# Kernel tuning notes

Hardware: AMD Instinct MI355X
Metric: run time of the kernel (lower is better)

The kernel has to match this reference:

```python
import jax, jax.numpy as jnp
import numpy as np

N_NODES = 50000
N_EDGES = 800000
IN_DIM = 96
OUT_DIM = 96
EDGE_DIM = 32
BN_EPS = 1e-5


def setup_inputs() -> dict:
    key = jax.random.key(0)
    ks = jax.random.split(key, 12)
    x = jax.random.normal(ks[0], (N_NODES, IN_DIM), dtype=jnp.float32)
    edge_index = jax.random.randint(ks[1], (2, N_EDGES), 0, N_NODES, dtype=jnp.int64)
    edge_attr = jax.random.normal(ks[2], (N_EDGES, EDGE_DIM), dtype=jnp.float32)
    # GINEConv edge projection Linear(edge_dim, in_dim)
    We = jax.random.normal(ks[3], (EDGE_DIM, IN_DIM), dtype=jnp.float32) / np.sqrt(EDGE_DIM)
    be = jnp.zeros((IN_DIM,), dtype=jnp.float32)
    # MLP: Linear(in_dim, out_dim) -> ReLU -> Linear(out_dim, out_dim)
    W1 = jax.random.normal(ks[4], (IN_DIM, OUT_DIM), dtype=jnp.float32) / np.sqrt(IN_DIM)
    b1 = jnp.zeros((OUT_DIM,), dtype=jnp.float32)
    W2 = jax.random.normal(ks[5], (OUT_DIM, OUT_DIM), dtype=jnp.float32) / np.sqrt(OUT_DIM)
    b2 = jnp.zeros((OUT_DIM,), dtype=jnp.float32)
    # BatchNorm1d affine params
    gamma = jnp.ones((OUT_DIM,), dtype=jnp.float32)
    beta = jnp.zeros((OUT_DIM,), dtype=jnp.float32)
    return {"x": x, "edge_index": edge_index, "edge_attr": edge_attr,
            "We": We, "be": be, "W1": W1, "b1": b1, "W2": W2, "b2": b2,
            "gamma": gamma, "beta": beta}


def reference(x, edge_index, edge_attr, We, be, W1, b1, W2, b2, gamma, beta):
    src = edge_index[0]  # x_j (message source)
    dst = edge_index[1]  # aggregation target
    # GINE message: ReLU(x_j + Lin(edge_attr)) per edge  [E, in_dim]
    msg = jax.nn.relu(x[src] + edge_attr @ We + be)
    # sum aggregation into dst nodes  [N, in_dim]
    aggr = jax.ops.segment_sum(msg, dst, num_segments=x.shape[0])
    # (1 + eps) * x + aggr, eps = 0 (GINEConv default)
    h = x + aggr
    # MLP: Linear -> ReLU -> Linear
    h = jax.nn.relu(h @ W1 + b1) @ W2 + b2
    # BatchNorm1d (training-mode batch statistics) + affine
    mean = jnp.mean(h, axis=0)
    var = jnp.mean(jnp.square(h - mean), axis=0)  # biased var, as torch BN uses
    h = (h - mean) * jax.lax.rsqrt(var + BN_EPS) * gamma + beta
    # ReLU (dropout is identity in eval / deterministic reference)
    return jax.nn.relu(h)
```

## Files before the change

kernel.cpp:

```cpp
#include <hip/hip_runtime.h>

typedef unsigned short ushort_t;
typedef unsigned int uint_t;
typedef __attribute__((ext_vector_type(8))) short bf16x8;
typedef __attribute__((ext_vector_type(4))) float f32x4;
typedef __attribute__((ext_vector_type(2))) float f32x2;

#define N_NODES 50000
#define N_EDGES 800000
#define BN_EPS 1e-5f

#define OFF_STATS 4800000
#define OFF_FLAG  4800192

#define SC_PAIR  0
#define SC_LEXCL 1600000
#define SC_DEG   1650016
#define SC_RANK  1700032
#define SC_BSUM  2500032

#define NB_SCAN 196
#define MTILE 64
#define NTILES ((N_NODES + MTILE - 1) / MTILE)

__device__ __forceinline__ ushort_t f2bf(float f) {
    uint_t u = __float_as_uint(f);
    uint_t r = ((u >> 16) & 1u) + 0x7fffu;
    return (ushort_t)((u + r) >> 16);
}

__global__ __launch_bounds__(256) void init_kernel(const int* __restrict__ ei,
                                                   int* __restrict__ flag,
                                                   int* __restrict__ deg,
                                                   float* __restrict__ stats) {
    const int gtid = blockIdx.x * 256 + threadIdx.x;
    const int nth = gridDim.x * 256;
    for (int i = gtid; i < N_NODES; i += nth) deg[i] = 0;
    if (gtid < 256) stats[gtid] = 0.f;
    if (blockIdx.x == 0) {
        __shared__ int s_any;
        if (threadIdx.x == 0) s_any = 0;
        __syncthreads();
        int nz = 0;
#pragma unroll
        for (int j = 0; j < 16; ++j) {
            const int p = 1 + 2 * (threadIdx.x * 16 + j) * 195;
            if (ei[p] != 0) nz = 1;
        }
        if (nz) atomicOr(&s_any, 1);
        __syncthreads();
        if (threadIdx.x == 0) *flag = s_any ? 0 : 1;
    }
}

__global__ __launch_bounds__(256) void hist_kernel(const int* __restrict__ ei,
                                                   const int* __restrict__ flag,
                                                   int* __restrict__ deg,
                                                   int* __restrict__ rank) {
    const int is64 = *flag;
    const int stride = gridDim.x * blockDim.x;
    for (int e = blockIdx.x * blockDim.x + threadIdx.x; e < N_EDGES; e += stride) {
        int s, d;
        if (is64) { s = ei[2 * e]; d = ei[2 * N_EDGES + 2 * e]; }
        else      { s = ei[e];     d = ei[N_EDGES + e]; }
        if ((uint_t)s < N_NODES && (uint_t)d < N_NODES)
            rank[e] = atomicAdd(&deg[d], 1);
    }
}

__global__ __launch_bounds__(256) void scanA_kernel(const int* __restrict__ deg,
                                                    int* __restrict__ lexcl,
                                                    int* __restrict__ bsum) {
    __shared__ int sd[256];
    const int tid = threadIdx.x;
    const int i = blockIdx.x * 256 + tid;
    const int v = (i < N_NODES) ? deg[i] : 0;
    sd[tid] = v;
    __syncthreads();
    for (int off = 1; off < 256; off <<= 1) {
        int u = (tid >= off) ? sd[tid - off] : 0;
        __syncthreads();
        sd[tid] += u;
        __syncthreads();
    }
    if (i < N_NODES) lexcl[i] = sd[tid] - v;
    if (tid == 255) bsum[blockIdx.x] = sd[255];
}

__device__ __forceinline__ void build_sbase(const int* __restrict__ bsum,
                                            int* sd, int* sbase, int* tot) {
    const int tid = threadIdx.x;
    const int v = (tid < NB_SCAN) ? bsum[tid] : 0;
    sd[tid] = v;
    __syncthreads();
    for (int off = 1; off < 256; off <<= 1) {
        int u = (tid >= off) ? sd[tid - off] : 0;
        __syncthreads();
        sd[tid] += u;
        __syncthreads();
    }
    if (tid < NB_SCAN) sbase[tid] = sd[tid] - v;
    if (tid == NB_SCAN - 1) *tot = sd[tid];
    __syncthreads();
}

__global__ __launch_bounds__(256) void scatter_kernel(const int* __restrict__ ei,
                                                      const int* __restrict__ flag,
                                                      const int* __restrict__ lexcl,
                                                      const int* __restrict__ bsum,
                                                      const int* __restrict__ rank,
                                                      int2* __restrict__ pair) {
    __shared__ int sd[256];
    __shared__ int sbase[NB_SCAN];
    __shared__ int tot;
    build_sbase(bsum, sd, sbase, &tot);

    const int is64 = *flag;
    const int stride = gridDim.x * blockDim.x;
    for (int e = blockIdx.x * blockDim.x + threadIdx.x; e < N_EDGES; e += stride) {
        int s, d;
        if (is64) { s = ei[2 * e]; d = ei[2 * N_EDGES + 2 * e]; }
        else      { s = ei[e];     d = ei[N_EDGES + e]; }
        if ((uint_t)s < N_NODES && (uint_t)d < N_NODES) {
            const int pos = sbase[d >> 8] + lexcl[d] + rank[e];
            pair[pos] = make_int2(e, s);
        }
    }
}

__global__ __launch_bounds__(256) void node_aggr_kernel(
    const float* __restrict__ x, const float* __restrict__ ea,
    const float* __restrict__ We, const float* __restrict__ be,
    const int2* __restrict__ pair, const int* __restrict__ lexcl,
    const int* __restrict__ bsum, float* __restrict__ hbuf) {
    __shared__ int sd[256];
    __shared__ int sbase[NB_SCAN];
    __shared__ int tot;
    build_sbase(bsum, sd, sbase, &tot);

    const int lane = threadIdx.x & 63;
    const int q = lane >> 4;
    const int t = lane & 15;
    const int wav = blockIdx.x * 4 + (threadIdx.x >> 6);
    const int nwav = gridDim.x * 4;

    bf16x8 Bf[6];
    float ben[6];
#pragma unroll
    for (int f = 0; f < 6; ++f) {
        const int n = t + 16 * f;
#pragma unroll
        for (int j = 0; j < 8; ++j) {
            const int k = q * 8 + j;
            Bf[f][j] = (short)f2bf(We[k * 96 + n]);
        }
        ben[f] = be[n];
    }

    for (int n = wav; n < N_NODES; n += nwav) {
        const int off = sbase[n >> 8] + lexcl[n];
        const int offn = (n + 1 == N_NODES) ? tot
                         : sbase[(n + 1) >> 8] + lexcl[n + 1];
        const int deg = offn - off;

        float part[6];
#pragma unroll
        for (int f = 0; f < 6; ++f) part[f] = 0.f;

        for (int c0 = 0; c0 < deg; c0 += 16) {
            const int rem = deg - c0;
            int eid_t = -1, src_t = -1;
            if (t < rem) {
                const int2 p = pair[off + c0 + t];
                eid_t = p.x;
                src_t = p.y;
            }
            bf16x8 A = {0, 0, 0, 0, 0, 0, 0, 0};
            if (eid_t >= 0) {
                const float* row = ea + (size_t)eid_t * 32 + q * 8;
                f32x4 a0 = *(const f32x4*)(row);
                f32x4 a1 = *(const f32x4*)(row + 4);
#pragma unroll
                for (int j = 0; j < 4; ++j) {
                    A[j] = (short)f2bf(a0[j]);
                    A[4 + j] = (short)f2bf(a1[j]);
                }
            }

            f32x4 acc[6];
#pragma unroll
            for (int f = 0; f < 6; ++f) {
                f32x4 z = {0.f, 0.f, 0.f, 0.f};
                acc[f] = __builtin_amdgcn_mfma_f32_16x16x32_bf16(A, Bf[f], z, 0, 0, 0);
            }

            int s_r[4];
#pragma unroll
            for (int r = 0; r < 4; ++r) s_r[r] = __shfl(src_t, q * 4 + r);

#pragma unroll
            for (int r = 0; r < 4; ++r) {
                const int m = q * 4 + r;
                if (m < rem) {
                    const float* xrow = x + (size_t)s_r[r] * 96;
#pragma unroll
                    for (int f = 0; f < 6; ++f) {
                        float v = acc[f][r] + ben[f] + xrow[t + 16 * f];
                        part[f] += v > 0.f ? v : 0.f;
                    }
                }
            }
        }

#pragma unroll
        for (int f = 0; f < 6; ++f) {
            part[f] += __shfl_xor(part[f], 16);
            part[f] += __shfl_xor(part[f], 32);
        }

        if (q == 0) {
            const float* xn = x + (size_t)n * 96;
            float* hn = hbuf + (size_t)n * 96;
#pragma unroll
            for (int f = 0; f < 6; ++f) {
                const int col = t + 16 * f;
                hn[col] = part[f] + xn[col];
            }
        }
    }
}

__global__ __launch_bounds__(256) void mlp_kernel(
    float* buf, const float* __restrict__ W1g, const float* __restrict__ b1g,
    const float* __restrict__ W2g, const float* __restrict__ b2g,
    float* __restrict__ stats) {
    __shared__ float Ws[96 * 96];
    __shared__ float hsT[96][68];

    const int tid = threadIdx.x;
    const int fg = tid & 15;
    const int ng = tid >> 4;
    const int n0 = blockIdx.x * MTILE;

    for (int i = tid; i < 96 * 96 / 4; i += 256)
        ((f32x4*)Ws)[i] = ((const f32x4*)W1g)[i];
    for (int i = tid; i < MTILE * 96 / 4; i += 256) {
        const int base = i * 4;
        const int nn = base / 96, k = base - nn * 96;
        f32x4 v = {0.f, 0.f, 0.f, 0.f};
        if (n0 + nn < N_NODES)
            v = *(const f32x4*)(buf + (size_t)(n0 + nn) * 96 + k);
        hsT[k][nn] = v[0]; hsT[k + 1][nn] = v[1];
        hsT[k + 2][nn] = v[2]; hsT[k + 3][nn] = v[3];
    }
    __syncthreads();

    float acc[4][6];
#pragma unroll
    for (int ff = 0; ff < 6; ++ff) {
        const float b = b1g[6 * fg + ff];
        acc[0][ff] = b; acc[1][ff] = b; acc[2][ff] = b; acc[3][ff] = b;
    }
    for (int k = 0; k < 96; ++k) {
        const f32x4 a = *(const f32x4*)&hsT[k][4 * ng];
        const float* wr = &Ws[k * 96 + 6 * fg];
        const f32x2 w01 = *(const f32x2*)(wr);
        const f32x2 w23 = *(const f32x2*)(wr + 2);
        const f32x2 w45 = *(const f32x2*)(wr + 4);
        const float w[6] = {w01[0], w01[1], w23[0], w23[1], w45[0], w45[1]};
#pragma unroll
        for (int nn = 0; nn < 4; ++nn)
#pragma unroll
            for (int ff = 0; ff < 6; ++ff) acc[nn][ff] += a[nn] * w[ff];
    }
    __syncthreads();

#pragma unroll
    for (int nn = 0; nn < 4; ++nn)
#pragma unroll
        for (int ff = 0; ff < 6; ++ff) {
            float v = acc[nn][ff];
            hsT[6 * fg + ff][4 * ng + nn] = v > 0.f ? v : 0.f;
        }
    for (int i = tid; i < 96 * 96 / 4; i += 256)
        ((f32x4*)Ws)[i] = ((const f32x4*)W2g)[i];
    __syncthreads();

#pragma unroll
    for (int ff = 0; ff < 6; ++ff) {
        const float b = b2g[6 * fg + ff];
        acc[0][ff] = b; acc[1][ff] = b; acc[2][ff] = b; acc[3][ff] = b;
    }
    for (int k = 0; k < 96; ++k) {
        const f32x4 a = *(const f32x4*)&hsT[k][4 * ng];
        const float* wr = &Ws[k * 96 + 6 * fg];
        const f32x2 w01 = *(const f32x2*)(wr);
        const f32x2 w23 = *(const f32x2*)(wr + 2);
        const f32x2 w45 = *(const f32x2*)(wr + 4);
        const float w[6] = {w01[0], w01[1], w23[0], w23[1], w45[0], w45[1]};
#pragma unroll
        for (int nn = 0; nn < 4; ++nn)
#pragma unroll
            for (int ff = 0; ff < 6; ++ff) acc[nn][ff] += a[nn] * w[ff];
    }

#pragma unroll
    for (int nn = 0; nn < 4; ++nn) {
        const int n = n0 + 4 * ng + nn;
        if (n < N_NODES) {
            float* o = buf + (size_t)n * 96 + 6 * fg;
            *(f32x2*)(o)     = (f32x2){acc[nn][0], acc[nn][1]};
            *(f32x2*)(o + 2) = (f32x2){acc[nn][2], acc[nn][3]};
            *(f32x2*)(o + 4) = (f32x2){acc[nn][4], acc[nn][5]};
        }
    }

    __syncthreads();
#pragma unroll
    for (int nn = 0; nn < 4; ++nn)
#pragma unroll
        for (int ff = 0; ff < 6; ++ff)
            hsT[6 * fg + ff][4 * ng + nn] = acc[nn][ff];
    __syncthreads();

    if (tid < 96) {
        int nmax = N_NODES - n0;
        if (nmax > MTILE) nmax = MTILE;
        float s = 0.f, s2 = 0.f;
        for (int n = 0; n < nmax; ++n) {
            const float v = hsT[tid][n];
            s += v; s2 += v * v;
        }
        atomicAdd(&stats[tid], s);
        atomicAdd(&stats[96 + tid], s2);
    }
}

__global__ __launch_bounds__(256) void bn_kernel(
    const float* __restrict__ h2, const float* __restrict__ stats,
    const float* __restrict__ gamma, const float* __restrict__ beta,
    float* __restrict__ out) {
    __shared__ float sc[96], sh[96];
    const int tid = threadIdx.x;
    if (tid < 96) {
        const float inv_n = 1.f / (float)N_NODES;
        const float mean = stats[tid] * inv_n;
        float var = stats[96 + tid] * inv_n - mean * mean;
        var = var > 0.f ? var : 0.f;
        const float s = gamma[tid] * rsqrtf(var + BN_EPS);
        sc[tid] = s;
        sh[tid] = beta[tid] - mean * s;
    }
    __syncthreads();
    const int total4 = N_NODES * 96 / 4;
    for (int i = blockIdx.x * blockDim.x + tid; i < total4;
         i += gridDim.x * blockDim.x) {
        f32x4 v = ((const f32x4*)h2)[i];
        const int jb = (i * 4) % 96;
#pragma unroll
        for (int c = 0; c < 4; ++c) {
            float u = v[c] * sc[jb + c] + sh[jb + c];
            v[c] = u > 0.f ? u : 0.f;
        }
        ((f32x4*)out)[i] = v;
    }
}

extern "C" void kernel_launch(void* const* d_in, const int* in_sizes, int n_in,
                              void* d_out, int out_size, void* d_ws,
                              size_t ws_size, hipStream_t stream) {
    const float* x     = (const float*)d_in[0];
    const int*   ei    = (const int*)d_in[1];
    const float* ea    = (const float*)d_in[2];
    const float* We    = (const float*)d_in[3];
    const float* be    = (const float*)d_in[4];
    const float* W1    = (const float*)d_in[5];
    const float* b1    = (const float*)d_in[6];
    const float* W2    = (const float*)d_in[7];
    const float* b2    = (const float*)d_in[8];
    const float* gamma = (const float*)d_in[9];
    const float* beta  = (const float*)d_in[10];
    float* out = (float*)d_out;

    float* ws    = (float*)d_ws;
    float* hbuf  = ws;
    float* stats = ws + OFF_STATS;
    int*   flagp = (int*)(ws + OFF_FLAG);

    int*  scratch = (int*)d_out;
    int2* pair    = (int2*)(scratch + SC_PAIR);
    int*  lexcl   = scratch + SC_LEXCL;
    int*  deg     = scratch + SC_DEG;
    int*  rank    = scratch + SC_RANK;
    int*  bsum    = scratch + SC_BSUM;

    init_kernel<<<NB_SCAN, 256, 0, stream>>>(ei, flagp, deg, stats);
    hist_kernel<<<1024, 256, 0, stream>>>(ei, flagp, deg, rank);
    scanA_kernel<<<NB_SCAN, 256, 0, stream>>>(deg, lexcl, bsum);
    scatter_kernel<<<1024, 256, 0, stream>>>(ei, flagp, lexcl, bsum, rank, pair);
    node_aggr_kernel<<<2048, 256, 0, stream>>>(x, ea, We, be, pair, lexcl,
                                               bsum, hbuf);
    mlp_kernel<<<NTILES, 256, 0, stream>>>(hbuf, W1, b1, W2, b2, stats);
    bn_kernel<<<1024, 256, 0, stream>>>(hbuf, stats, gamma, beta, out);
}
```

Baseline: 390.0 us.

## Split aggregation and MLP launches into chunks; replicate BN stats accumulators

The node aggregation kernel is now launched four times over quarter node ranges, and the MLP kernel twice over half tile ranges. Separately, the BN statistics are spread over eight replicated accumulator slots to reduce atomic contention, and the BN kernel sums them. The chunked launches add launch overhead and leave each quarter-range launch with many idle waves (2048 blocks for 12500 nodes), so the intent behind the split is unclear. It may be a probe of per-chunk behaviour.

```diff
diff --git a/kernel.cpp b/kernel.cpp
--- a/kernel.cpp
+++ b/kernel.cpp
@@ -11,7 +11,8 @@
 #define BN_EPS 1e-5f
 
 #define OFF_STATS 4800000
-#define OFF_FLAG  4800192
+#define OFF_FLAG  4801536
+#define NREP 8
 
 #define SC_PAIR  0
 #define SC_LEXCL 1600000
@@ -36,7 +37,7 @@
     const int gtid = blockIdx.x * 256 + threadIdx.x;
     const int nth = gridDim.x * 256;
     for (int i = gtid; i < N_NODES; i += nth) deg[i] = 0;
-    if (gtid < 256) stats[gtid] = 0.f;
+    if (gtid < NREP * 192) stats[gtid] = 0.f;
     if (blockIdx.x == 0) {
         __shared__ int s_any;
         if (threadIdx.x == 0) s_any = 0;
@@ -132,7 +133,8 @@
     const float* __restrict__ x, const float* __restrict__ ea,
     const float* __restrict__ We, const float* __restrict__ be,
     const int2* __restrict__ pair, const int* __restrict__ lexcl,
-    const int* __restrict__ bsum, float* __restrict__ hbuf) {
+    const int* __restrict__ bsum, float* __restrict__ hbuf,
+    int n0, int n1) {
     __shared__ int sd[256];
     __shared__ int sbase[NB_SCAN];
     __shared__ int tot;
@@ -157,7 +159,7 @@
         ben[f] = be[n];
     }
 
-    for (int n = wav; n < N_NODES; n += nwav) {
+    for (int n = n0 + wav; n < n1; n += nwav) {
         const int off = sbase[n >> 8] + lexcl[n];
         const int offn = (n + 1 == N_NODES) ? tot
                          : sbase[(n + 1) >> 8] + lexcl[n + 1];
@@ -233,14 +235,14 @@
 __global__ __launch_bounds__(256) void mlp_kernel(
     float* buf, const float* __restrict__ W1g, const float* __restrict__ b1g,
     const float* __restrict__ W2g, const float* __restrict__ b2g,
-    float* __restrict__ stats) {
+    float* __restrict__ stats, int tb) {
     __shared__ float Ws[96 * 96];
     __shared__ float hsT[96][68];
 
     const int tid = threadIdx.x;
     const int fg = tid & 15;
     const int ng = tid >> 4;
-    const int n0 = blockIdx.x * MTILE;
+    const int n0 = (tb + blockIdx.x) * MTILE;
 
     for (int i = tid; i < 96 * 96 / 4; i += 256)
         ((f32x4*)Ws)[i] = ((const f32x4*)W1g)[i];
@@ -331,8 +333,9 @@
             const float v = hsT[tid][n];
             s += v; s2 += v * v;
         }
-        atomicAdd(&stats[tid], s);
-        atomicAdd(&stats[96 + tid], s2);
+        float* st = stats + (blockIdx.x & (NREP - 1)) * 192;
+        atomicAdd(&st[tid], s);
+        atomicAdd(&st[96 + tid], s2);
     }
 }
 
@@ -343,9 +346,15 @@
     __shared__ float sc[96], sh[96];
     const int tid = threadIdx.x;
     if (tid < 96) {
+        float s1 = 0.f, s2 = 0.f;
+#pragma unroll
+        for (int r = 0; r < NREP; ++r) {
+            s1 += stats[r * 192 + tid];
+            s2 += stats[r * 192 + 96 + tid];
+        }
         const float inv_n = 1.f / (float)N_NODES;
-        const float mean = stats[tid] * inv_n;
-        float var = stats[96 + tid] * inv_n - mean * mean;
+        const float mean = s1 * inv_n;
+        float var = s2 * inv_n - mean * mean;
         var = var > 0.f ? var : 0.f;
         const float s = gamma[tid] * rsqrtf(var + BN_EPS);
         sc[tid] = s;
@@ -399,7 +408,15 @@
     scanA_kernel<<<NB_SCAN, 256, 0, stream>>>(deg, lexcl, bsum);
     scatter_kernel<<<1024, 256, 0, stream>>>(ei, flagp, lexcl, bsum, rank, pair);
     node_aggr_kernel<<<2048, 256, 0, stream>>>(x, ea, We, be, pair, lexcl,
-                                               bsum, hbuf);
-    mlp_kernel<<<NTILES, 256, 0, stream>>>(hbuf, W1, b1, W2, b2, stats);
+                                               bsum, hbuf, 0, 12500);
+    node_aggr_kernel<<<2048, 256, 0, stream>>>(x, ea, We, be, pair, lexcl,
+                                               bsum, hbuf, 12500, 25000);
+    node_aggr_kernel<<<2048, 256, 0, stream>>>(x, ea, We, be, pair, lexcl,
+                                               bsum, hbuf, 25000, 37500);
+    node_aggr_kernel<<<2048, 256, 0, stream>>>(x, ea, We, be, pair, lexcl,
+                                               bsum, hbuf, 37500, 50000);
+    mlp_kernel<<<NTILES / 2, 256, 0, stream>>>(hbuf, W1, b1, W2, b2, stats, 0);
+    mlp_kernel<<<NTILES - NTILES / 2, 256, 0, stream>>>(hbuf, W1, b1, W2, b2,
+                                                        stats, NTILES / 2);
     bn_kernel<<<1024, 256, 0, stream>>>(hbuf, stats, gamma, beta, out);
 }
```

New measurement: 407.4 us. 1.04x slower.
